# Kernel optimization log

Measured on AMD Instinct MI355X. Metric: run time of the kernel, lower is better.

Reference implementation:

```python
import jax, jax.numpy as jnp
import numpy as np

TOP_K = 2

def setup_inputs() -> dict:
    key = jax.random.key(0)
    k1, k2 = jax.random.split(key)
    hidden_states = jax.random.normal(k1, (4, 4096, 4096), dtype=jnp.float32)
    # nn.Linear(dim, num_experts, bias=False) weight: [num_experts, dim]
    router_weight = jax.random.normal(k2, (64, 4096), dtype=jnp.float32) * (4096 ** -0.5)
    return {"hidden_states": hidden_states, "router_weight": router_weight}

def reference(hidden_states, router_weight):
    # logits: (batch, seq, num_experts)
    logits = jnp.einsum('bsd,ed->bse', hidden_states, router_weight)
    # Shazeer et al. 2017 Eq. 1: softmax over the kept top-k logits.
    topk_logits, topk_indices = jax.lax.top_k(logits, TOP_K)
    topk_scores = jax.nn.softmax(topk_logits, axis=-1)  # (batch, seq, top_k)
    return topk_scores, topk_indices
```

## Files before the change

kernel.cpp:

```cpp
#include <hip/hip_runtime.h>
#include <math.h>

#define TOKENS 16384
#define DIM    4096
#define NEXP   64
#define KSPLIT 4
#define KSLICE (DIM / KSPLIT)
#define BK     32
#define NCHUNK (KSLICE / BK)
#define TB     128
#define NCHUNK_G (DIM / BK)

typedef _Float16 f16x8 __attribute__((ext_vector_type(8)));
typedef float    f32x4 __attribute__((ext_vector_type(4)));

#define MFMA16(a, b, c) __builtin_amdgcn_mfma_f32_16x16x32_f16((a), (b), (c), 0, 0, 0)

__device__ __forceinline__ void gload16(const void* g, void* l) {
    __builtin_amdgcn_global_load_lds(
        (const __attribute__((address_space(1))) void*)g,
        (__attribute__((address_space(3))) void*)l, 16, 0, 0);
}

__global__ __launch_bounds__(256)
void pack_w_kernel(const float* __restrict__ w, uint4* __restrict__ wpk) {
    const int lane = threadIdx.x & 63;
    const int t    = threadIdx.x >> 6;
    const int c    = blockIdx.x;
    const int e    = 16 * t + (lane & 15);
    const int k0   = 32 * c + 8 * (lane >> 4);

    const float* src = w + (size_t)e * DIM + k0;
    const float4 v0 = *(const float4*)(src);
    const float4 v1 = *(const float4*)(src + 4);
    const float xs[8] = {v0.x, v0.y, v0.z, v0.w, v1.x, v1.y, v1.z, v1.w};

    f16x8 hi, lo;
#pragma unroll
    for (int j = 0; j < 8; ++j) {
        const float xv = xs[j];
        _Float16 h = (_Float16)xv;
        float hf = (float)h;
        if (fabsf(xv) < 6.103515625e-05f) {
            h = (_Float16)0.f; hf = 0.f;
        }
        hi[j] = h;
        lo[j] = (_Float16)((xv - hf) * 65536.f);
    }

    wpk[(size_t)c * 512 + (2 * t + 0) * 64 + lane] = *(const uint4*)&hi;
    wpk[(size_t)c * 512 + (2 * t + 1) * 64 + lane] = *(const uint4*)&lo;
}

__device__ __forceinline__ void split_a(const f32x4 lo, const f32x4 hi,
                                        f16x8& ah, f16x8& al) {
    const float xs[8] = {lo[0], lo[1], lo[2], lo[3], hi[0], hi[1], hi[2], hi[3]};
#pragma unroll
    for (int j = 0; j < 8; ++j) {
        const float xv = xs[j];
        const _Float16 h = (_Float16)xv;
        ah[j] = h;
        al[j] = (_Float16)((xv - (float)h) * 65536.f);
    }
}

__device__ __forceinline__ void fma3(const f16x8 ah, const f16x8 al,
                                     const f16x8 bh, const f16x8 bl,
                                     f32x4& a1, f32x4& a2) {
    a1 = MFMA16(ah, bh, a1);
    a2 = MFMA16(ah, bl, a2);
    a2 = MFMA16(al, bh, a2);
}

__global__ __launch_bounds__(512)
__attribute__((amdgpu_waves_per_eu(4, 4)))
void router_gemm_kernel(const float* __restrict__ x,
                        const uint4* __restrict__ wpk,
                        float* __restrict__ part) {
    __shared__ uint4 lds[5120];

    const int tid  = threadIdx.x;
    const int lane = tid & 63;
    const int wv   = tid >> 6;
    const int tf   = wv >> 1;
    const int et   = wv & 1;
    const int bid  = blockIdx.x;
    const int ks   = bid & (KSPLIT - 1);
    const int token0 = (bid >> 2) * TB;

    const int rl = lane >> 3;
    const int sb = (lane & 7) ^ rl;
    const float* xsrc0 = x + (size_t)(token0 + 16 * wv + rl) * DIM
                       + ks * KSLICE + 4 * sb;
    const float* xsrc1 = xsrc0 + (size_t)8 * DIM;
    const uint4* bsrc = wpk + (size_t)(ks * NCHUNK) * 512 + wv * 64 + lane;

    const int xib = ((lane >> 3) & 1) * 64 + (lane & 7) * 8;
    const int xk0 = (2 * (lane >> 4)    ) ^ (lane & 7);
    const int xk1 = (2 * (lane >> 4) + 1) ^ (lane & 7);

    f32x4 a1[2][2], a2[2][2];
    const f32x4 zero = {0.f, 0.f, 0.f, 0.f};
#pragma unroll
    for (int f = 0; f < 2; ++f)
#pragma unroll
        for (int e = 0; e < 2; ++e) { a1[f][e] = zero; a2[f][e] = zero; }

    gload16(xsrc0,          &lds[0 * 1024 + wv * 128]);
    gload16(xsrc0 + BK,     &lds[1 * 1024 + wv * 128]);
    gload16(xsrc1,          &lds[0 * 1024 + wv * 128 + 64]);
    gload16(xsrc1 + BK,     &lds[1 * 1024 + wv * 128 + 64]);
    gload16(bsrc,           &lds[4096 + 0 * 512 + wv * 64]);

#pragma unroll 1
    for (int c = 0; c < NCHUNK; ++c) {
        {
            const int cb = (c + 1) & (NCHUNK - 1);
            gload16(bsrc + (size_t)cb * 512,
                    &lds[4096 + ((c + 1) & 1) * 512 + wv * 64]);
        }
        if (!(c & 1)) {
            const int c2 = (c + 2) & (NCHUNK - 1);
            const int c3 = (c + 3) & (NCHUNK - 1);
            uint4* d2 = &lds[((c + 2) & 3) * 1024 + wv * 128];
            uint4* d3 = &lds[((c + 3) & 3) * 1024 + wv * 128];
            gload16(xsrc0 + c2 * BK, d2);
            gload16(xsrc0 + c3 * BK, d3);
            gload16(xsrc1 + c2 * BK, d2 + 64);
            gload16(xsrc1 + c3 * BK, d3 + 64);
        }
        asm volatile("s_waitcnt vmcnt(5)" ::: "memory");
        __builtin_amdgcn_s_barrier();

        const uint4* Xr = &lds[(c & 3) * 1024];
        const uint4* Br = &lds[4096 + (c & 1) * 512];

        f16x8 ah0, al0, ah1, al1;
        {
            const int b0 = (2 * tf + 0) * 128 + xib;
            const int b1 = (2 * tf + 1) * 128 + xib;
            const f32x4 A0l = *(const f32x4*)&Xr[b0 + xk0];
            const f32x4 A0h = *(const f32x4*)&Xr[b0 + xk1];
            const f32x4 A1l = *(const f32x4*)&Xr[b1 + xk0];
            const f32x4 A1h = *(const f32x4*)&Xr[b1 + xk1];
            split_a(A0l, A0h, ah0, al0);
            split_a(A1l, A1h, ah1, al1);
        }
        const f16x8 bh0 = *(const f16x8*)&Br[(4 * et + 0) * 64 + lane];
        const f16x8 bl0 = *(const f16x8*)&Br[(4 * et + 1) * 64 + lane];
        const f16x8 bh1 = *(const f16x8*)&Br[(4 * et + 2) * 64 + lane];
        const f16x8 bl1 = *(const f16x8*)&Br[(4 * et + 3) * 64 + lane];

        __builtin_amdgcn_s_setprio(1);
        fma3(ah0, al0, bh0, bl0, a1[0][0], a2[0][0]);
        fma3(ah0, al0, bh1, bl1, a1[0][1], a2[0][1]);
        fma3(ah1, al1, bh0, bl0, a1[1][0], a2[1][0]);
        fma3(ah1, al1, bh1, bl1, a1[1][1], a2[1][1]);
        __builtin_amdgcn_s_setprio(0);

        asm volatile("s_waitcnt lgkmcnt(0)" ::: "memory");
        __builtin_amdgcn_s_barrier();
    }

#pragma unroll
    for (int f = 0; f < 2; ++f) {
#pragma unroll
        for (int e = 0; e < 2; ++e) {
            const f32x4 v = a1[f][e] + a2[f][e] * (1.f / 65536.f);
            float* pout = part
                + ((size_t)ks * TOKENS + token0 + (2 * tf + f) * 16
                   + 4 * (lane >> 4)) * NEXP
                + 16 * (2 * et + e) + (lane & 15);
#pragma unroll
            for (int rr = 0; rr < 4; ++rr)
                pout[(size_t)rr * NEXP] = v[rr];
        }
    }
}

__global__ __launch_bounds__(256)
void topk_kernel(const float* __restrict__ part, float* __restrict__ out) {
    const int lane  = threadIdx.x & 63;
    const int wv    = threadIdx.x >> 6;
    const int token = blockIdx.x * 4 + wv;

    float logit = 0.f;
#pragma unroll
    for (int s = 0; s < KSPLIT; ++s)
        logit += part[((size_t)s * TOKENS + token) * NEXP + lane];

    float v1 = logit; int i1 = lane;
#pragma unroll
    for (int off = 32; off > 0; off >>= 1) {
        const float ov = __shfl_xor(v1, off);
        const int   oi = __shfl_xor(i1, off);
        if (ov > v1 || (ov == v1 && oi < i1)) { v1 = ov; i1 = oi; }
    }
    float v2 = (lane == i1) ? -INFINITY : logit; int i2 = lane;
#pragma unroll
    for (int off = 32; off > 0; off >>= 1) {
        const float ov = __shfl_xor(v2, off);
        const int   oi = __shfl_xor(i2, off);
        if (ov > v2 || (ov == v2 && oi < i2)) { v2 = ov; i2 = oi; }
    }

    if (lane == 0) {
        const float e = expf(v2 - v1);
        const float r = 1.f / (1.f + e);
        out[2 * token + 0] = r;
        out[2 * token + 1] = e * r;
        out[2 * TOKENS + 2 * token + 0] = (float)i1;
        out[2 * TOKENS + 2 * token + 1] = (float)i2;
    }
}

extern "C" void kernel_launch(void* const* d_in, const int* in_sizes, int n_in,
                              void* d_out, int out_size, void* d_ws, size_t ws_size,
                              hipStream_t stream) {
    const float* x = (const float*)d_in[0];
    const float* w = (const float*)d_in[1];
    float* out  = (float*)d_out;
    float* part = (float*)d_ws;
    uint4* wpk = (uint4*)((char*)d_ws + (size_t)KSPLIT * TOKENS * NEXP * sizeof(float));

    pack_w_kernel<<<NCHUNK_G, 256, 0, stream>>>(w, wpk);
    router_gemm_kernel<<<(TOKENS / TB) * KSPLIT, 512, 0, stream>>>(x, wpk, part);
    topk_kernel<<<TOKENS / 4, 256, 0, stream>>>(part, out);
}
```

Measured before the change: 385.2 us.

## Halve token tile and stage X in 4-chunk groups with deeper B prefetch

Cuts the token tile per block from 128 to 64, which doubles the grid. X is now staged a whole group of four K-chunks at a time into double-buffered LDS, and B is prefetched up to four chunks ahead into an 8-slot ring with graded vmcnt waits. The aim is more blocks in flight and fewer, larger global-to-LDS transfers, so memory latency hides better. In exchange each wave does half the MFMA work per X load, LDS use grows, and the waves_per_eu hint is removed.

```diff
diff --git a/kernel.cpp b/kernel.cpp
--- a/kernel.cpp
+++ b/kernel.cpp
@@ -8,7 +8,9 @@
 #define KSLICE (DIM / KSPLIT)
 #define BK     32
 #define NCHUNK (KSLICE / BK)
-#define TB     128
+#define GROUP  4
+#define NGROUP (NCHUNK / GROUP)
+#define TB     64
 #define NCHUNK_G (DIM / BK)
 
 typedef _Float16 f16x8 __attribute__((ext_vector_type(8)));
@@ -73,11 +75,10 @@
 }
 
 __global__ __launch_bounds__(512)
-__attribute__((amdgpu_waves_per_eu(4, 4)))
 void router_gemm_kernel(const float* __restrict__ x,
                         const uint4* __restrict__ wpk,
                         float* __restrict__ part) {
-    __shared__ uint4 lds[5120];
+    __shared__ uint4 lds[8192];
 
     const int tid  = threadIdx.x;
     const int lane = tid & 63;
@@ -86,95 +87,89 @@
     const int et   = wv & 1;
     const int bid  = blockIdx.x;
     const int ks   = bid & (KSPLIT - 1);
-    const int token0 = (bid >> 2) * TB;
-
-    const int rl = lane >> 3;
-    const int sb = (lane & 7) ^ rl;
-    const float* xsrc0 = x + (size_t)(token0 + 16 * wv + rl) * DIM
-                       + ks * KSLICE + 4 * sb;
-    const float* xsrc1 = xsrc0 + (size_t)8 * DIM;
+    const int t0   = (bid >> 2) * TB;
+
+    const int half = lane >> 5;
+    const int li   = lane & 31;
+    const float* xs_[4];
+#pragma unroll
+    for (int i = 0; i < 4; ++i) {
+        const int rlow = 2 * i + half;
+        xs_[i] = x + (size_t)(t0 + 8 * wv + rlow) * DIM + ks * KSLICE
+               + 4 * (li ^ rlow);
+    }
     const uint4* bsrc = wpk + (size_t)(ks * NCHUNK) * 512 + wv * 64 + lane;
 
-    const int xib = ((lane >> 3) & 1) * 64 + (lane & 7) * 8;
-    const int xk0 = (2 * (lane >> 4)    ) ^ (lane & 7);
-    const int xk1 = (2 * (lane >> 4) + 1) ^ (lane & 7);
-
-    f32x4 a1[2][2], a2[2][2];
+    const int R   = 16 * tf + (lane & 15);
+    const int hi4 = (lane >> 4) & 3;
+    const int s3  = lane & 7;
+
+    f32x4 a1[2], a2[2];
     const f32x4 zero = {0.f, 0.f, 0.f, 0.f};
-#pragma unroll
-    for (int f = 0; f < 2; ++f)
-#pragma unroll
-        for (int e = 0; e < 2; ++e) { a1[f][e] = zero; a2[f][e] = zero; }
-
-    gload16(xsrc0,          &lds[0 * 1024 + wv * 128]);
-    gload16(xsrc0 + BK,     &lds[1 * 1024 + wv * 128]);
-    gload16(xsrc1,          &lds[0 * 1024 + wv * 128 + 64]);
-    gload16(xsrc1 + BK,     &lds[1 * 1024 + wv * 128 + 64]);
-    gload16(bsrc,           &lds[4096 + 0 * 512 + wv * 64]);
+    a1[0] = a1[1] = zero; a2[0] = a2[1] = zero;
+
+    auto STAGE_X = [&](int g) {
+        uint4* d = &lds[(g & 1) * 2048 + (8 * wv) * 32];
+        const int go = (g & (NGROUP - 1)) * (GROUP * BK);
+#pragma unroll
+        for (int i = 0; i < 4; ++i)
+            gload16(xs_[i] + go, d + i * 64);
+    };
+    auto STAGE_B = [&](int cb) {
+        const int c = cb & (NCHUNK - 1);
+        gload16(bsrc + (size_t)c * 512, &lds[4096 + (c & 7) * 512 + wv * 64]);
+    };
+
+    STAGE_X(0);
+    STAGE_B(0);
+    asm volatile("s_waitcnt vmcnt(0)" ::: "memory");
+    __builtin_amdgcn_s_barrier();
+
+#define CHUNK_O(o, VMASM)                                                     \
+    do {                                                                      \
+        asm volatile(VMASM ::: "memory");                                     \
+        __builtin_amdgcn_s_barrier();                                         \
+        const uint4* Xr = &lds[(g & 1) * 2048 + R * 32];                      \
+        const uint4* Br = &lds[4096 + ((4 * g + (o)) & 7) * 512];             \
+        const f32x4 Alo = *(const f32x4*)&Xr[(8 * (o) + 2 * hi4 + 0) ^ s3];   \
+        const f32x4 Ahi = *(const f32x4*)&Xr[(8 * (o) + 2 * hi4 + 1) ^ s3];   \
+        f16x8 ah, al;                                                         \
+        split_a(Alo, Ahi, ah, al);                                            \
+        const f16x8 bh0 = *(const f16x8*)&Br[(4 * et + 0) * 64 + lane];       \
+        const f16x8 bl0 = *(const f16x8*)&Br[(4 * et + 1) * 64 + lane];       \
+        const f16x8 bh1 = *(const f16x8*)&Br[(4 * et + 2) * 64 + lane];       \
+        const f16x8 bl1 = *(const f16x8*)&Br[(4 * et + 3) * 64 + lane];       \
+        __builtin_amdgcn_s_setprio(1);                                        \
+        fma3(ah, al, bh0, bl0, a1[0], a2[0]);                                 \
+        fma3(ah, al, bh1, bl1, a1[1], a2[1]);                                 \
+        __builtin_amdgcn_s_setprio(0);                                        \
+        asm volatile("s_waitcnt lgkmcnt(0)" ::: "memory");                    \
+        __builtin_amdgcn_s_barrier();                                         \
+    } while (0)
 
 #pragma unroll 1
-    for (int c = 0; c < NCHUNK; ++c) {
-        {
-            const int cb = (c + 1) & (NCHUNK - 1);
-            gload16(bsrc + (size_t)cb * 512,
-                    &lds[4096 + ((c + 1) & 1) * 512 + wv * 64]);
-        }
-        if (!(c & 1)) {
-            const int c2 = (c + 2) & (NCHUNK - 1);
-            const int c3 = (c + 3) & (NCHUNK - 1);
-            uint4* d2 = &lds[((c + 2) & 3) * 1024 + wv * 128];
-            uint4* d3 = &lds[((c + 3) & 3) * 1024 + wv * 128];
-            gload16(xsrc0 + c2 * BK, d2);
-            gload16(xsrc0 + c3 * BK, d3);
-            gload16(xsrc1 + c2 * BK, d2 + 64);
-            gload16(xsrc1 + c3 * BK, d3 + 64);
-        }
-        asm volatile("s_waitcnt vmcnt(5)" ::: "memory");
-        __builtin_amdgcn_s_barrier();
-
-        const uint4* Xr = &lds[(c & 3) * 1024];
-        const uint4* Br = &lds[4096 + (c & 1) * 512];
-
-        f16x8 ah0, al0, ah1, al1;
-        {
-            const int b0 = (2 * tf + 0) * 128 + xib;
-            const int b1 = (2 * tf + 1) * 128 + xib;
-            const f32x4 A0l = *(const f32x4*)&Xr[b0 + xk0];
-            const f32x4 A0h = *(const f32x4*)&Xr[b0 + xk1];
-            const f32x4 A1l = *(const f32x4*)&Xr[b1 + xk0];
-            const f32x4 A1h = *(const f32x4*)&Xr[b1 + xk1];
-            split_a(A0l, A0h, ah0, al0);
-            split_a(A1l, A1h, ah1, al1);
-        }
-        const f16x8 bh0 = *(const f16x8*)&Br[(4 * et + 0) * 64 + lane];
-        const f16x8 bl0 = *(const f16x8*)&Br[(4 * et + 1) * 64 + lane];
-        const f16x8 bh1 = *(const f16x8*)&Br[(4 * et + 2) * 64 + lane];
-        const f16x8 bl1 = *(const f16x8*)&Br[(4 * et + 3) * 64 + lane];
-
-        __builtin_amdgcn_s_setprio(1);
-        fma3(ah0, al0, bh0, bl0, a1[0][0], a2[0][0]);
-        fma3(ah0, al0, bh1, bl1, a1[0][1], a2[0][1]);
-        fma3(ah1, al1, bh0, bl0, a1[1][0], a2[1][0]);
-        fma3(ah1, al1, bh1, bl1, a1[1][1], a2[1][1]);
-        __builtin_amdgcn_s_setprio(0);
-
-        asm volatile("s_waitcnt lgkmcnt(0)" ::: "memory");
-        __builtin_amdgcn_s_barrier();
-    }
-
-#pragma unroll
-    for (int f = 0; f < 2; ++f) {
-#pragma unroll
-        for (int e = 0; e < 2; ++e) {
-            const f32x4 v = a1[f][e] + a2[f][e] * (1.f / 65536.f);
-            float* pout = part
-                + ((size_t)ks * TOKENS + token0 + (2 * tf + f) * 16
-                   + 4 * (lane >> 4)) * NEXP
-                + 16 * (2 * et + e) + (lane & 15);
-#pragma unroll
-            for (int rr = 0; rr < 4; ++rr)
-                pout[(size_t)rr * NEXP] = v[rr];
-        }
+    for (int g = 0; g < NGROUP; ++g) {
+        STAGE_B(4 * g + 1);
+        STAGE_B(4 * g + 2);
+        STAGE_B(4 * g + 3);
+        STAGE_B(4 * g + 4);
+        STAGE_X(g + 1);
+        CHUNK_O(0, "s_waitcnt vmcnt(8)");
+        CHUNK_O(1, "s_waitcnt vmcnt(7)");
+        CHUNK_O(2, "s_waitcnt vmcnt(6)");
+        CHUNK_O(3, "s_waitcnt vmcnt(5)");
+    }
+#undef CHUNK_O
+
+#pragma unroll
+    for (int e = 0; e < 2; ++e) {
+        const f32x4 v = a1[e] + a2[e] * (1.f / 65536.f);
+        float* pout = part
+            + ((size_t)ks * TOKENS + t0 + 16 * tf + 4 * (lane >> 4)) * NEXP
+            + 16 * (2 * et + e) + (lane & 15);
+#pragma unroll
+        for (int rr = 0; rr < 4; ++rr)
+            pout[(size_t)rr * NEXP] = v[rr];
     }
 }
 
```

New measurement: 371.5 us. -3.6%, faster.
